# Performance work log

Hardware: AMD Instinct MI355X
Metric: run time of the kernel (lower is better)

The kernel has to match this reference:

```python
import jax, jax.numpy as jnp
import numpy as np

N_NODES = 100000
N_EDGES = 2000000


def _init_mlp(key, dims, scale=0.05):
    Ws, bs = [], []
    ks = jax.random.split(key, len(dims) - 1)
    for k, di, do in zip(ks, dims[:-1], dims[1:]):
        Ws.append(jax.random.normal(k, (di, do), dtype=jnp.float32) * scale)
        bs.append(jnp.zeros((do,), dtype=jnp.float32))
    return Ws, bs


def setup_inputs() -> dict:
    key = jax.random.key(0)
    ks = jax.random.split(key, 7)
    d = {
        "t": jax.random.uniform(ks[0], (1,), dtype=jnp.float32),
        "x": jax.random.normal(ks[1], (N_NODES, 4), dtype=jnp.float32),
        "Ofixed": jax.random.normal(ks[2], (N_NODES, 2), dtype=jnp.float32),
        "src_idx": jax.random.randint(ks[3], (N_EDGES,), 0, N_NODES, dtype=jnp.int32),
        "tgt_idx": jax.random.randint(ks[4], (N_EDGES,), 0, N_NODES, dtype=jnp.int32),
    }
    # fR: (2*d_O+1)=13 -> [150]*4 -> 50 ; fO: 50 -> [100] -> 4
    R_Ws, R_bs = _init_mlp(ks[5], [13, 150, 150, 150, 150, 50])
    O_Ws, O_bs = _init_mlp(ks[6], [50, 100, 4])
    for i, (W, b) in enumerate(zip(R_Ws, R_bs)):
        d[f"fR_W{i}"] = W
        d[f"fR_b{i}"] = b
    for i, (W, b) in enumerate(zip(O_Ws, O_bs)):
        d[f"fO_W{i}"] = W
        d[f"fO_b{i}"] = b
    return d


def _mlp(h, Ws, bs):
    # hidden layers with ReLU, linear output (matches MLP in the torch code)
    for W, b in zip(Ws[:-1], bs[:-1]):
        h = jax.nn.relu(h @ W + b)
    return h @ Ws[-1] + bs[-1]


def reference(t, x, Ofixed, src_idx, tgt_idx,
              fR_W0, fR_b0, fR_W1, fR_b1, fR_W2, fR_b2, fR_W3, fR_b3, fR_W4, fR_b4,
              fO_W0, fO_b0, fO_W1, fO_b1):
    O = jnp.concatenate([x, Ofixed], axis=1)            # [N, d_O]
    # Msrc.T @ O and Mtgt.T @ O with 0/1 incidence matrices == gathers
    Rsrc = O[src_idx]                                   # [M, d_O]
    Rtgt = O[tgt_idx]                                   # [M, d_O]
    tt = jnp.broadcast_to(t.reshape(1, 1).astype(O.dtype), (src_idx.shape[0], 1))
    R_prime = jnp.concatenate([Rsrc, Rtgt, tt], axis=1)  # [M, 2*d_O+1]
    E = _mlp(R_prime, [fR_W0, fR_W1, fR_W2, fR_W3, fR_W4],
             [fR_b0, fR_b1, fR_b2, fR_b3, fR_b4])        # [M, d_E]
    # Mtgt @ E == scatter-add of edge messages onto target nodes
    E_prime = jax.ops.segment_sum(E, tgt_idx, num_segments=x.shape[0])  # [N, d_E]
    P = _mlp(E_prime, [fO_W0, fO_W1], [fO_b0, fO_b1])    # [N, d_P]
    return P
```

## Files before the change

### kernel.cpp

```cpp
#include <hip/hip_runtime.h>
#include <hip/hip_bf16.h>

typedef unsigned short u16;
typedef unsigned int u32;
typedef __attribute__((ext_vector_type(8))) short short8;
typedef __attribute__((ext_vector_type(4))) float f32x4;

constexpr int SA     = 192;
constexpr int BLK_E  = 128;
constexpr int NTHR   = 256;
constexpr int CHUNK  = 512;
constexpr int WSLOT  = 50 * CHUNK;
constexpr size_t WS_HDR   = 262144;

constexpr int Ls (int s) { return s == 0 ? 0 : (s <= 15 ? 1 + (s - 1) / 5 : 4); }
constexpr int Kss(int s) { return s == 0 ? 0 : (s <= 15 ? (s - 1) % 5 : s - 16); }

__device__ __forceinline__ int aswz(int row, int elem) {
    return row * SA + (elem ^ ((row & 7) << 3));
}

__device__ __forceinline__ u16 f2bf(float f) {
    union { float f; unsigned u; } c; c.f = f;
    return (u16)((c.u + 0x7fffu + ((c.u >> 16) & 1u)) >> 16);
}
__device__ __forceinline__ unsigned pk_bf16(float a, float b) {
    float2 f; f.x = a; f.y = b;
    __hip_bfloat162 h = __float22bfloat162_rn(f);
    return *(unsigned*)&h;
}

__device__ __forceinline__ int kperm(int kp) {
    if (kp < 64)  return (kp & 3) * 16 + (kp >> 2);
    if (kp < 128) { const int m = kp - 64; return (5 + (m & 3)) * 16 + (m >> 2); }
    if (kp < 144) return 4 * 16 + (kp - 128);
    if (kp < 160) return 9 * 16 + (kp - 144);
    return 1 << 30;
}

__global__ void prep_all(const float* __restrict__ W0, const float* __restrict__ W1,
                         const float* __restrict__ W2, const float* __restrict__ W3,
                         const float* __restrict__ W4,
                         const float* __restrict__ B0, const float* __restrict__ B1,
                         const float* __restrict__ B2, const float* __restrict__ B3,
                         const float* __restrict__ B4,
                         u16* __restrict__ Wt, u32* __restrict__ cursor, int n_nodes)
{
    const int l = blockIdx.y;
    if (l == 5) {
        for (int idx = blockIdx.x * blockDim.x + threadIdx.x; idx < n_nodes;
             idx += gridDim.x * blockDim.x)
            cursor[idx] = 0u;
        return;
    }
    const float* W; const float* B; int DI, DO; bool perm;
    if      (l == 0) { W = W0; B = B0; DI = 13;  DO = 150; perm = false; }
    else if (l == 1) { W = W1; B = B1; DI = 150; DO = 150; perm = true;  }
    else if (l == 2) { W = W2; B = B2; DI = 150; DO = 150; perm = true;  }
    else if (l == 3) { W = W3; B = B3; DI = 150; DO = 150; perm = true;  }
    else             { W = W4; B = B4; DI = 150; DO = 50;  perm = true;  }
    const int kbias = (l == 0) ? 13 : 150;
    u16* dst = Wt + (size_t)l * WSLOT;
    for (int idx = blockIdx.x * blockDim.x + threadIdx.x; idx < WSLOT;
         idx += gridDim.x * blockDim.x) {
        const int chunk = idx / CHUNK;
        const int within = idx - chunk * CHUNK;
        const int lane = within >> 3, e = within & 7;
        const int ks = chunk / 10, j = chunk - ks * 10;
        const int c = lane & 15, q = lane >> 4;
        const int n = j * 16 + c;
        const int kphys = ks * 32 + q * 8 + e;
        const int klog = perm ? kperm(kphys) : kphys;
        float v = 0.f;
        if (n < DO) {
            if (klog < DI)          v = W[klog * DO + n];
            else if (klog == kbias) v = B[n];
        }
        dst[idx] = f2bf(v);
    }
}

__device__ __forceinline__ void loadHalfH(const u16* __restrict__ Wt, int h,
                                          int lane, short8* buf)
{
    int l, ks, g, nch;
    if (h < 32) { const int s = h >> 1; l = Ls(s); ks = Kss(s); g = h & 1; nch = 5; }
    else        { l = 4; ks = h - 32; g = 0; nch = 4; }
    const u16* base = Wt + (size_t)l * WSLOT + (size_t)(ks * 10 + g * 5) * CHUNK
                         + lane * 8;
#pragma unroll
    for (int jj = 0; jj < 5; ++jj)
        if (jj < nch) buf[jj] = *(const short8*)&base[jj * CHUNK];
}

__device__ __forceinline__ void epilogueF(u16* act, int ebase, int col, int quad,
                                          f32x4 (&acc)[2][10])
{
#pragma unroll
    for (int mtl = 0; mtl < 2; ++mtl)
#pragma unroll
        for (int r = 0; r < 4; ++r) {
            const int row = ebase + mtl * 16 + quad * 4 + r;
            uint2 p0, p1;
            p0.x = pk_bf16(fmaxf(acc[mtl][0][r], 0.f), fmaxf(acc[mtl][1][r], 0.f));
            p0.y = pk_bf16(fmaxf(acc[mtl][2][r], 0.f), fmaxf(acc[mtl][3][r], 0.f));
            p1.x = pk_bf16(fmaxf(acc[mtl][5][r], 0.f), fmaxf(acc[mtl][6][r], 0.f));
            p1.y = pk_bf16(fmaxf(acc[mtl][7][r], 0.f), fmaxf(acc[mtl][8][r], 0.f));
            *(uint2*)&act[aswz(row, col * 4)]      = p0;
            *(uint2*)&act[aswz(row, 64 + col * 4)] = p1;
            act[aswz(row, 128 + col)] =
                (u16)pk_bf16(fmaxf(acc[mtl][4][r], 0.f), 0.f);
            u16 sv = (u16)pk_bf16(fmaxf(acc[mtl][9][r], 0.f), 0.f);
            if (col == 6) sv = 0x3F80;
            act[aswz(row, 144 + col)] = sv;
        }
}

__global__ void hist_kernel(const int* __restrict__ tgt, u32* __restrict__ cnt,
                            int n_edges)
{
    const int e = blockIdx.x * blockDim.x + threadIdx.x;
    if (e < n_edges) atomicAdd(&cnt[tgt[e]], 1u);
}

__global__ void scan1_kernel(const u32* __restrict__ cnt, u32* __restrict__ offs,
                             u32* __restrict__ bsum, int n)
{
    __shared__ u32 s[256];
    const int i = blockIdx.x * 256 + threadIdx.x;
    const u32 v = (i < n) ? cnt[i] : 0u;
    s[threadIdx.x] = v; __syncthreads();
#pragma unroll
    for (int d = 1; d < 256; d <<= 1) {
        const u32 t = (threadIdx.x >= d) ? s[threadIdx.x - d] : 0u;
        __syncthreads();
        s[threadIdx.x] += t;
        __syncthreads();
    }
    if (i < n) offs[i] = s[threadIdx.x] - v;
    if (threadIdx.x == 255) bsum[blockIdx.x] = s[255];
}

__global__ void scan2_kernel(u32* __restrict__ bsum, int nb)
{
    __shared__ u32 s[512];
    const int i = threadIdx.x;
    const u32 v = (i < nb) ? bsum[i] : 0u;
    s[i] = v; __syncthreads();
#pragma unroll
    for (int d = 1; d < 512; d <<= 1) {
        const u32 t = (i >= d) ? s[i - d] : 0u;
        __syncthreads();
        s[i] += t;
        __syncthreads();
    }
    if (i < nb) bsum[i] = s[i] - v;
}

__global__ void scan3_kernel(u32* __restrict__ offs, const u32* __restrict__ bsum,
                             u32* __restrict__ cursor, int n, int n_edges)
{
    const int i = blockIdx.x * 256 + threadIdx.x;
    if (i < n) {
        const u32 o = offs[i] + bsum[blockIdx.x];
        offs[i] = o;
        cursor[i] = o;
    }
    if (blockIdx.x == 0 && threadIdx.x == 0) offs[n] = (u32)n_edges;
}

__global__ void perm_kernel(const int* __restrict__ src, const int* __restrict__ tgt,
                            u32* __restrict__ cursor, int2* __restrict__ sg,
                            int n_edges)
{
    const int e = blockIdx.x * blockDim.x + threadIdx.x;
    if (e < n_edges) {
        const int g = tgt[e];
        const u32 pos = atomicAdd(&cursor[g], 1u);
        sg[pos] = make_int2(src[e], g);
    }
}

__global__ __launch_bounds__(NTHR, 3) void edge_kernel(
    const float* __restrict__ t, const float* __restrict__ x, const float* __restrict__ Ofx,
    const int2* __restrict__ sgp,
    const u16* __restrict__ Wt,
    float* __restrict__ Ep, int n_edges)
{
    __shared__ __align__(16) u16 act[BLK_E * SA];
    __shared__ int tgt_s[BLK_E];

    const int tid   = threadIdx.x;
    const int lane  = tid & 63;
    const int wv    = tid >> 6;
    const int ebase = wv * 32;
    const int col   = lane & 15;
    const int quad  = lane >> 4;

    if (lane < 32) {
        const int e = ebase + lane;
        const long long ge = (long long)blockIdx.x * BLK_E + e;
        const bool valid = ge < n_edges;
        const int2 sg = valid ? sgp[ge] : make_int2(0, 0);
        const int g = valid ? sg.y : -1;
        const float4 xs = valid ? *(const float4*)&x[(size_t)sg.x * 4] : float4{0, 0, 0, 0};
        const float2 os = valid ? *(const float2*)&Ofx[(size_t)sg.x * 2] : float2{0, 0};
        const float4 xg = valid ? *(const float4*)&x[(size_t)sg.y * 4] : float4{0, 0, 0, 0};
        const float2 og = valid ? *(const float2*)&Ofx[(size_t)sg.y * 2] : float2{0, 0};
        const float tv = valid ? t[0] : 0.f;
        uint4 w0, w1;
        w0.x = pk_bf16(xs.x, xs.y); w0.y = pk_bf16(xs.z, xs.w);
        w0.z = pk_bf16(os.x, os.y); w0.w = pk_bf16(xg.x, xg.y);
        w1.x = pk_bf16(xg.z, xg.w); w1.y = pk_bf16(og.x, og.y);
        w1.z = pk_bf16(tv, 1.0f);   w1.w = 0u;
        *(uint4*)&act[aswz(e, 0)]  = w0;
        *(uint4*)&act[aswz(e, 8)]  = w1;
        *(uint4*)&act[aswz(e, 16)] = uint4{0, 0, 0, 0};
        *(uint4*)&act[aswz(e, 24)] = uint4{0, 0, 0, 0};
        tgt_s[e] = g;
    }

    const f32x4 z = {0.f, 0.f, 0.f, 0.f};
    f32x4 acc[2][10];
    short8 Wb[3][5];
    short8 Af[2];

    loadHalfH(Wt, 0, lane, Wb[0]);
    loadHalfH(Wt, 1, lane, Wb[1]);
    loadHalfH(Wt, 2, lane, Wb[2]);

#pragma unroll
    for (int s = 0; s <= 15; ++s) {
        const int ks = Kss(s);
        const bool first = (s == 0) || (ks == 0);
        const int h0 = 2 * s, h1 = 2 * s + 1;
#pragma unroll
        for (int mtl = 0; mtl < 2; ++mtl)
            Af[mtl] = *(const short8*)&act[aswz(ebase + mtl * 16 + col,
                                                ks * 32 + quad * 8)];
#pragma unroll
        for (int jj = 0; jj < 5; ++jj)
#pragma unroll
            for (int mtl = 0; mtl < 2; ++mtl)
                acc[mtl][jj] = __builtin_amdgcn_mfma_f32_16x16x32_bf16(
                    Af[mtl], Wb[h0 % 3][jj], first ? z : acc[mtl][jj], 0, 0, 0);
        loadHalfH(Wt, h0 + 3, lane, Wb[h0 % 3]);
#pragma unroll
        for (int jj = 0; jj < 5; ++jj)
#pragma unroll
            for (int mtl = 0; mtl < 2; ++mtl)
                acc[mtl][5 + jj] = __builtin_amdgcn_mfma_f32_16x16x32_bf16(
                    Af[mtl], Wb[h1 % 3][jj], first ? z : acc[mtl][5 + jj], 0, 0, 0);
        loadHalfH(Wt, h1 + 3, lane, Wb[h1 % 3]);
        if (s == 0 || ks == 4)
            epilogueF(act, ebase, col, quad, acc);
    }

    f32x4 acc4[2][4];
#pragma unroll
    for (int ks4 = 0; ks4 < 5; ++ks4) {
        const int h = 32 + ks4;
#pragma unroll
        for (int mtl = 0; mtl < 2; ++mtl)
            Af[mtl] = *(const short8*)&act[aswz(ebase + mtl * 16 + col,
                                                ks4 * 32 + quad * 8)];
#pragma unroll
        for (int jj = 0; jj < 4; ++jj)
#pragma unroll
            for (int mtl = 0; mtl < 2; ++mtl)
                acc4[mtl][jj] = __builtin_amdgcn_mfma_f32_16x16x32_bf16(
                    Af[mtl], Wb[h % 3][jj], (ks4 == 0) ? z : acc4[mtl][jj], 0, 0, 0);
        if (h + 3 <= 36) loadHalfH(Wt, h + 3, lane, Wb[h % 3]);
    }

    float* actF = (float*)&act[ebase * SA];
#pragma unroll
    for (int mtl = 0; mtl < 2; ++mtl)
#pragma unroll
        for (int jj = 0; jj < 4; ++jj) {
            const int n = jj * 16 + col;
            if (n < 50) {
#pragma unroll
                for (int r = 0; r < 4; ++r)
                    actF[(mtl * 16 + quad * 4 + r) * 52 + n] = acc4[mtl][jj][r];
            }
        }
    if (lane < 50) {
        const int c = lane;
        int   cur = tgt_s[ebase];
        float a   = 0.f;
        for (int r = 0; r < 32; ++r) {
            const int   g = tgt_s[ebase + r];
            const float v = actF[r * 52 + c];
            if (g != cur) {
                if (cur >= 0) atomicAdd(&Ep[(size_t)cur * 50 + c], a);
                a = 0.f; cur = g;
            }
            a += v;
        }
        if (cur >= 0) atomicAdd(&Ep[(size_t)cur * 50 + c], a);
    }
}

template<int DI, int DO, bool RELU>
__device__ __forceinline__ void mlp_layer_t(
    const float* __restrict__ W, const float* __restrict__ B,
    float (*in)[64], float (*out)[64], int tid)
{
    const int et = tid & 15;
    const int jt = tid >> 4;
    constexpr int NG = (DO + 15) / 16;

    float acc0[NG], acc1[NG], acc2[NG], acc3[NG];
#pragma unroll
    for (int g = 0; g < NG; ++g) {
        const int j = jt + 16 * g;
        const float bb = (j < DO) ? B[j] : 0.f;
        acc0[g] = bb; acc1[g] = bb; acc2[g] = bb; acc3[g] = bb;
    }
    for (int k = 0; k < DI; ++k) {
        const float4 a = *(const float4*)&in[k][et * 4];
#pragma unroll
        for (int g = 0; g < NG; ++g) {
            const int j = jt + 16 * g;
            const float wv = (j < DO) ? W[k * DO + j] : 0.f;
            acc0[g] = fmaf(a.x, wv, acc0[g]);
            acc1[g] = fmaf(a.y, wv, acc1[g]);
            acc2[g] = fmaf(a.z, wv, acc2[g]);
            acc3[g] = fmaf(a.w, wv, acc3[g]);
        }
    }
#pragma unroll
    for (int g = 0; g < NG; ++g) {
        const int j = jt + 16 * g;
        if (j < DO) {
            float4 v; v.x = acc0[g]; v.y = acc1[g]; v.z = acc2[g]; v.w = acc3[g];
            if (RELU) {
                v.x = fmaxf(v.x, 0.f); v.y = fmaxf(v.y, 0.f);
                v.z = fmaxf(v.z, 0.f); v.w = fmaxf(v.w, 0.f);
            }
            *(float4*)&out[j][et * 4] = v;
        }
    }
}

__global__ __launch_bounds__(256, 2) void node_kernel(
    const float* __restrict__ Ep,
    const float* __restrict__ W0, const float* __restrict__ B0,
    const float* __restrict__ W1, const float* __restrict__ B1,
    float* __restrict__ P, int n_nodes)
{
    __shared__ float bufA[104][64];
    __shared__ float bufB[104][64];
    const int tid = threadIdx.x;
    const int n0  = blockIdx.x * 64;

    for (int idx = tid; idx < 64 * 50; idx += 256) {
        const int e = idx / 50;
        const int k = idx - e * 50;
        const int n = n0 + e;
        bufA[k][e] = (n < n_nodes) ? Ep[(size_t)n * 50 + k] : 0.f;
    }
    __syncthreads();
    mlp_layer_t<50, 100, true >(W0, B0, bufA, bufB, tid); __syncthreads();
    mlp_layer_t<100, 4, false>(W1, B1, bufB, bufA, tid); __syncthreads();
    for (int idx = tid; idx < 64 * 4; idx += 256) {
        const int e = idx & 63;
        const int j = idx >> 6;
        const int n = n0 + e;
        if (n < n_nodes) P[(size_t)n * 4 + j] = bufA[j][e];
    }
}

extern "C" void kernel_launch(void* const* d_in, const int* in_sizes, int n_in,
                              void* d_out, int out_size, void* d_ws, size_t ws_size,
                              hipStream_t stream)
{
    const float* t   = (const float*)d_in[0];
    const float* x   = (const float*)d_in[1];
    const float* Ofx = (const float*)d_in[2];
    const int*   src = (const int*)d_in[3];
    const int*   tgt = (const int*)d_in[4];
    const float* W0  = (const float*)d_in[5];  const float* B0 = (const float*)d_in[6];
    const float* W1  = (const float*)d_in[7];  const float* B1 = (const float*)d_in[8];
    const float* W2  = (const float*)d_in[9];  const float* B2 = (const float*)d_in[10];
    const float* W3  = (const float*)d_in[11]; const float* B3 = (const float*)d_in[12];
    const float* W4  = (const float*)d_in[13]; const float* B4 = (const float*)d_in[14];
    const float* OW0 = (const float*)d_in[15]; const float* OB0 = (const float*)d_in[16];
    const float* OW1 = (const float*)d_in[17]; const float* OB1 = (const float*)d_in[18];

    const int n_nodes = in_sizes[1] / 4;
    const int n_edges = in_sizes[3];

    auto align256 = [](size_t v) { return (v + 255) & ~(size_t)255; };
    char* ws = (char*)d_ws;
    const size_t copy_elems = (size_t)n_nodes * 50;
    size_t o = 0;
    u16*   Wt       = (u16*)(ws + o);  o = WS_HDR;
    float* Ep       = (float*)(ws + o); o = align256(o + copy_elems * sizeof(float));
    u32*   offs     = (u32*)(ws + o);  o = align256(o + (size_t)(n_nodes + 1) * 4);
    u32*   cursor   = (u32*)(ws + o);  o = align256(o + (size_t)n_nodes * 4);
    u32*   bsum     = (u32*)(ws + o);  o = align256(o + 512 * 4);
    int2*  sg_perm  = (int2*)(ws + o); o = align256(o + (size_t)n_edges * 8);

    const int NB  = (n_nodes + 255) / 256;
    const int EBK = (n_edges + 255) / 256;

    prep_all<<<dim3(32, 6), 256, 0, stream>>>(W0, W1, W2, W3, W4,
                                              B0, B1, B2, B3, B4, Wt,
                                              cursor, n_nodes);
    hipMemsetAsync(Ep, 0, copy_elems * sizeof(float), stream);

    hist_kernel <<<EBK, 256, 0, stream>>>(tgt, cursor, n_edges);
    scan1_kernel<<<NB, 256, 0, stream>>>(cursor, offs, bsum, n_nodes);
    scan2_kernel<<<1, 512, 0, stream>>>(bsum, NB);
    scan3_kernel<<<NB, 256, 0, stream>>>(offs, bsum, cursor, n_nodes, n_edges);
    perm_kernel <<<EBK, 256, 0, stream>>>(src, tgt, cursor, sg_perm, n_edges);

    edge_kernel<<<(n_edges + BLK_E - 1) / BLK_E, NTHR, 0, stream>>>(
        t, x, Ofx, sg_perm, Wt, Ep, n_edges);

    node_kernel<<<(n_nodes + 63) / 64, 256, 0, stream>>>(
        Ep, OW0, OB0, OW1, OB1, (float*)d_out, n_nodes);
}
```

Baseline: 870.6 us.

## Shrink LDS row stride, drop swizzle, double-buffer weights, shuffle target ids

Cuts the activation row stride from 192 to 160 bf16 elements and removes the XOR swizzle on shared-memory addresses, which reduces LDS use per block. Weight prefetch drops from triple to double buffering to free registers. Per-edge target ids now stay in registers and are read with wave shuffles instead of a shared array, and the segmented reduction loads its values in batches of eight. The goal is higher occupancy and less LDS traffic, at the cost of possible bank conflicts without the swizzle and a shorter prefetch distance that may expose global-load latency.

```diff
diff --git a/kernel.cpp b/kernel.cpp
--- a/kernel.cpp
+++ b/kernel.cpp
@@ -6,7 +6,7 @@
 typedef __attribute__((ext_vector_type(8))) short short8;
 typedef __attribute__((ext_vector_type(4))) float f32x4;
 
-constexpr int SA     = 192;
+constexpr int SA     = 160;
 constexpr int BLK_E  = 128;
 constexpr int NTHR   = 256;
 constexpr int CHUNK  = 512;
@@ -15,10 +15,6 @@
 
 constexpr int Ls (int s) { return s == 0 ? 0 : (s <= 15 ? 1 + (s - 1) / 5 : 4); }
 constexpr int Kss(int s) { return s == 0 ? 0 : (s <= 15 ? (s - 1) % 5 : s - 16); }
-
-__device__ __forceinline__ int aswz(int row, int elem) {
-    return row * SA + (elem ^ ((row & 7) << 3));
-}
 
 __device__ __forceinline__ u16 f2bf(float f) {
     union { float f; unsigned u; } c; c.f = f;
@@ -101,18 +97,18 @@
 #pragma unroll
         for (int r = 0; r < 4; ++r) {
             const int row = ebase + mtl * 16 + quad * 4 + r;
+            u16* rp = &act[row * SA];
             uint2 p0, p1;
             p0.x = pk_bf16(fmaxf(acc[mtl][0][r], 0.f), fmaxf(acc[mtl][1][r], 0.f));
             p0.y = pk_bf16(fmaxf(acc[mtl][2][r], 0.f), fmaxf(acc[mtl][3][r], 0.f));
             p1.x = pk_bf16(fmaxf(acc[mtl][5][r], 0.f), fmaxf(acc[mtl][6][r], 0.f));
             p1.y = pk_bf16(fmaxf(acc[mtl][7][r], 0.f), fmaxf(acc[mtl][8][r], 0.f));
-            *(uint2*)&act[aswz(row, col * 4)]      = p0;
-            *(uint2*)&act[aswz(row, 64 + col * 4)] = p1;
-            act[aswz(row, 128 + col)] =
-                (u16)pk_bf16(fmaxf(acc[mtl][4][r], 0.f), 0.f);
+            *(uint2*)&rp[col * 4]      = p0;
+            *(uint2*)&rp[64 + col * 4] = p1;
+            rp[128 + col] = (u16)pk_bf16(fmaxf(acc[mtl][4][r], 0.f), 0.f);
             u16 sv = (u16)pk_bf16(fmaxf(acc[mtl][9][r], 0.f), 0.f);
             if (col == 6) sv = 0x3F80;
-            act[aswz(row, 144 + col)] = sv;
+            rp[144 + col] = sv;
         }
 }
 
@@ -188,7 +184,6 @@
     float* __restrict__ Ep, int n_edges)
 {
     __shared__ __align__(16) u16 act[BLK_E * SA];
-    __shared__ int tgt_s[BLK_E];
 
     const int tid   = threadIdx.x;
     const int lane  = tid & 63;
@@ -197,12 +192,13 @@
     const int col   = lane & 15;
     const int quad  = lane >> 4;
 
+    int gval = -1;
     if (lane < 32) {
         const int e = ebase + lane;
         const long long ge = (long long)blockIdx.x * BLK_E + e;
         const bool valid = ge < n_edges;
         const int2 sg = valid ? sgp[ge] : make_int2(0, 0);
-        const int g = valid ? sg.y : -1;
+        gval = valid ? sg.y : -1;
         const float4 xs = valid ? *(const float4*)&x[(size_t)sg.x * 4] : float4{0, 0, 0, 0};
         const float2 os = valid ? *(const float2*)&Ofx[(size_t)sg.x * 2] : float2{0, 0};
         const float4 xg = valid ? *(const float4*)&x[(size_t)sg.y * 4] : float4{0, 0, 0, 0};
@@ -213,45 +209,43 @@
         w0.z = pk_bf16(os.x, os.y); w0.w = pk_bf16(xg.x, xg.y);
         w1.x = pk_bf16(xg.z, xg.w); w1.y = pk_bf16(og.x, og.y);
         w1.z = pk_bf16(tv, 1.0f);   w1.w = 0u;
-        *(uint4*)&act[aswz(e, 0)]  = w0;
-        *(uint4*)&act[aswz(e, 8)]  = w1;
-        *(uint4*)&act[aswz(e, 16)] = uint4{0, 0, 0, 0};
-        *(uint4*)&act[aswz(e, 24)] = uint4{0, 0, 0, 0};
-        tgt_s[e] = g;
+        u16* rp = &act[e * SA];
+        *(uint4*)&rp[0]  = w0;
+        *(uint4*)&rp[8]  = w1;
+        *(uint4*)&rp[16] = uint4{0, 0, 0, 0};
+        *(uint4*)&rp[24] = uint4{0, 0, 0, 0};
     }
 
     const f32x4 z = {0.f, 0.f, 0.f, 0.f};
     f32x4 acc[2][10];
-    short8 Wb[3][5];
+    short8 Wb[2][5];
     short8 Af[2];
 
     loadHalfH(Wt, 0, lane, Wb[0]);
     loadHalfH(Wt, 1, lane, Wb[1]);
-    loadHalfH(Wt, 2, lane, Wb[2]);
 
 #pragma unroll
     for (int s = 0; s <= 15; ++s) {
         const int ks = Kss(s);
         const bool first = (s == 0) || (ks == 0);
-        const int h0 = 2 * s, h1 = 2 * s + 1;
 #pragma unroll
         for (int mtl = 0; mtl < 2; ++mtl)
-            Af[mtl] = *(const short8*)&act[aswz(ebase + mtl * 16 + col,
-                                                ks * 32 + quad * 8)];
+            Af[mtl] = *(const short8*)&act[(ebase + mtl * 16 + col) * SA
+                                           + ks * 32 + quad * 8];
 #pragma unroll
         for (int jj = 0; jj < 5; ++jj)
 #pragma unroll
             for (int mtl = 0; mtl < 2; ++mtl)
                 acc[mtl][jj] = __builtin_amdgcn_mfma_f32_16x16x32_bf16(
-                    Af[mtl], Wb[h0 % 3][jj], first ? z : acc[mtl][jj], 0, 0, 0);
-        loadHalfH(Wt, h0 + 3, lane, Wb[h0 % 3]);
+                    Af[mtl], Wb[0][jj], first ? z : acc[mtl][jj], 0, 0, 0);
+        loadHalfH(Wt, 2 * s + 2, lane, Wb[0]);
 #pragma unroll
         for (int jj = 0; jj < 5; ++jj)
 #pragma unroll
             for (int mtl = 0; mtl < 2; ++mtl)
                 acc[mtl][5 + jj] = __builtin_amdgcn_mfma_f32_16x16x32_bf16(
-                    Af[mtl], Wb[h1 % 3][jj], first ? z : acc[mtl][5 + jj], 0, 0, 0);
-        loadHalfH(Wt, h1 + 3, lane, Wb[h1 % 3]);
+                    Af[mtl], Wb[1][jj], first ? z : acc[mtl][5 + jj], 0, 0, 0);
+        loadHalfH(Wt, 2 * s + 3, lane, Wb[1]);
         if (s == 0 || ks == 4)
             epilogueF(act, ebase, col, quad, acc);
     }
@@ -262,15 +256,15 @@
         const int h = 32 + ks4;
 #pragma unroll
         for (int mtl = 0; mtl < 2; ++mtl)
-            Af[mtl] = *(const short8*)&act[aswz(ebase + mtl * 16 + col,
-                                                ks4 * 32 + quad * 8)];
+            Af[mtl] = *(const short8*)&act[(ebase + mtl * 16 + col) * SA
+                                           + ks4 * 32 + quad * 8];
 #pragma unroll
         for (int jj = 0; jj < 4; ++jj)
 #pragma unroll
             for (int mtl = 0; mtl < 2; ++mtl)
                 acc4[mtl][jj] = __builtin_amdgcn_mfma_f32_16x16x32_bf16(
-                    Af[mtl], Wb[h % 3][jj], (ks4 == 0) ? z : acc4[mtl][jj], 0, 0, 0);
-        if (h + 3 <= 36) loadHalfH(Wt, h + 3, lane, Wb[h % 3]);
+                    Af[mtl], Wb[h & 1][jj], (ks4 == 0) ? z : acc4[mtl][jj], 0, 0, 0);
+        if (h + 2 <= 36) loadHalfH(Wt, h + 2, lane, Wb[h & 1]);
     }
 
     float* actF = (float*)&act[ebase * SA];
@@ -287,16 +281,23 @@
         }
     if (lane < 50) {
         const int c = lane;
-        int   cur = tgt_s[ebase];
+        int   cur = __shfl(gval, 0);
         float a   = 0.f;
-        for (int r = 0; r < 32; ++r) {
-            const int   g = tgt_s[ebase + r];
-            const float v = actF[r * 52 + c];
-            if (g != cur) {
-                if (cur >= 0) atomicAdd(&Ep[(size_t)cur * 50 + c], a);
-                a = 0.f; cur = g;
+#pragma unroll
+        for (int rb = 0; rb < 4; ++rb) {
+            float vb[8];
+#pragma unroll
+            for (int j = 0; j < 8; ++j)
+                vb[j] = actF[(rb * 8 + j) * 52 + c];
+#pragma unroll
+            for (int j = 0; j < 8; ++j) {
+                const int g = __shfl(gval, rb * 8 + j);
+                if (g != cur) {
+                    if (cur >= 0) atomicAdd(&Ep[(size_t)cur * 50 + c], a);
+                    a = 0.f; cur = g;
+                }
+                a += vb[j];
             }
-            a += v;
         }
         if (cur >= 0) atomicAdd(&Ep[(size_t)cur * 50 + c], a);
     }
```

Result: no change. 881.2 us (+1.2%).
